# Kernel optimization log

Hardware: AMD Instinct MI355X
Metric: run time of the kernel (lower is better)

## Reference

```python
import jax, jax.numpy as jnp
import numpy as np

N = 25000      # number of target nodes
K = 32         # sampled neighbor fanout
F_IN = 256
F_OUT = 256


def setup_inputs() -> dict:
    key = jax.random.key(0)
    k1, k2, k3, k4 = jax.random.split(key, 4)
    x = jax.random.normal(k1, (N, F_IN), dtype=jnp.float32)
    neigh = jax.random.randint(k2, (N, K), 0, N, dtype=jnp.int64)
    # Linear(in_feats, out_feats) parameters
    W = jax.random.normal(k3, (F_IN, F_OUT), dtype=jnp.float32) / np.sqrt(F_IN)
    b = jax.random.normal(k4, (F_OUT,), dtype=jnp.float32) * 0.01
    return {"x": x, "neigh": neigh, "W": W, "b": b}


def reference(x, neigh, W, b):
    # Gather neighbor features: [N, K, F_IN]
    h = x[neigh]
    # Linear + ReLU transform on each neighbor feature
    h = jax.nn.relu(jnp.einsum('nkf,fo->nko', h, W) + b)
    # Element-wise max-pool across the neighbor set -> [N, F_OUT]
    return jnp.max(h, axis=1)
```

## Files before the change

### kernel.cpp

```cpp
#include <hip/hip_runtime.h>
#include <hip/hip_bf16.h>

#define N_NODES 25000
#define KFAN    32
#define FIN     256
#define FOUT    256

typedef float  f32x4  __attribute__((ext_vector_type(4)));
typedef short  s16x8  __attribute__((ext_vector_type(8)));

__device__ __forceinline__ ushort f2bf(float f) {
    unsigned int u = __float_as_uint(f);
    u += 0x7fffu + ((u >> 16) & 1u);
    return (ushort)(u >> 16);
}
__device__ __forceinline__ unsigned int pack2(float a, float b) {
    return (unsigned int)f2bf(a) | ((unsigned int)f2bf(b) << 16);
}

__global__ __launch_bounds__(256) void transpose_w(
    const float* __restrict__ W, ushort* __restrict__ Wt)
{
    __shared__ float ls[32][33];
    const int bid = blockIdx.x;
    const int kt  = bid & 7;
    const int nt  = bid >> 3;
    const int t   = threadIdx.x;

    {
        int kl = t >> 3, n4 = (t & 7) * 4;
        float4 v = *(const float4*)(W + (size_t)(kt * 32 + kl) * FOUT + nt * 32 + n4);
        ls[kl][n4 + 0] = v.x; ls[kl][n4 + 1] = v.y;
        ls[kl][n4 + 2] = v.z; ls[kl][n4 + 3] = v.w;
    }
    __syncthreads();
    {
        int nl = t >> 3, k4 = (t & 7) * 4;
        ushort4 o;
        o.x = f2bf(ls[k4 + 0][nl]);
        o.y = f2bf(ls[k4 + 1][nl]);
        o.z = f2bf(ls[k4 + 2][nl]);
        o.w = f2bf(ls[k4 + 3][nl]);
        *(ushort4*)(Wt + (size_t)(nt * 32 + nl) * FIN + kt * 32 + k4) = o;
    }
}

__global__ __launch_bounds__(256) void gemm_mfma(
    const float*  __restrict__ x,
    const ushort* __restrict__ Wt,
    const float*  __restrict__ bias,
    ushort*       __restrict__ y)
{
    __shared__ ushort As[64][72];

    const int tid  = threadIdx.x;
    const int lane = tid & 63;
    const int wv   = tid >> 6;
    const int l16  = lane & 15;
    const int q    = lane >> 4;
    const int row0 = blockIdx.x * 64;
    const int n0   = blockIdx.y * 128 + wv * 32;

    f32x4 acc[4][2];
    #pragma unroll
    for (int i = 0; i < 4; ++i)
        #pragma unroll
        for (int j = 0; j < 2; ++j) acc[i][j] = (f32x4)0.f;

    const int r    = tid >> 2;
    const int kcol = (tid & 3) * 16;

    for (int kc = 0; kc < FIN; kc += 64) {
        float4 v0 = make_float4(0.f,0.f,0.f,0.f), v1 = v0, v2 = v0, v3 = v0;
        int gr = row0 + r;
        if (gr < N_NODES) {
            const float* p = x + (size_t)gr * FIN + kc + kcol;
            v0 = *(const float4*)p;
            v1 = *(const float4*)(p + 4);
            v2 = *(const float4*)(p + 8);
            v3 = *(const float4*)(p + 12);
        }
        uint4 pa, pb;
        pa.x = pack2(v0.x, v0.y); pa.y = pack2(v0.z, v0.w);
        pa.z = pack2(v1.x, v1.y); pa.w = pack2(v1.z, v1.w);
        pb.x = pack2(v2.x, v2.y); pb.y = pack2(v2.z, v2.w);
        pb.z = pack2(v3.x, v3.y); pb.w = pack2(v3.z, v3.w);
        *(uint4*)&As[r][kcol]     = pa;
        *(uint4*)&As[r][kcol + 8] = pb;
        __syncthreads();

        #pragma unroll
        for (int kk = 0; kk < 64; kk += 32) {
            const int k0 = kk + q * 8;
            s16x8 a[4], b[2];
            #pragma unroll
            for (int mt = 0; mt < 4; ++mt)
                a[mt] = *(const s16x8*)&As[mt * 16 + l16][k0];
            #pragma unroll
            for (int ct = 0; ct < 2; ++ct)
                b[ct] = *(const s16x8*)(Wt + (size_t)(n0 + ct * 16 + l16) * FIN + kc + k0);
            #pragma unroll
            for (int mt = 0; mt < 4; ++mt)
                #pragma unroll
                for (int ct = 0; ct < 2; ++ct)
                    acc[mt][ct] = __builtin_amdgcn_mfma_f32_16x16x32_bf16(a[mt], b[ct], acc[mt][ct], 0, 0, 0);
        }
        __syncthreads();
    }

    #pragma unroll
    for (int ct = 0; ct < 2; ++ct) {
        const int col = n0 + ct * 16 + l16;
        const float bv = bias[col];
        #pragma unroll
        for (int mt = 0; mt < 4; ++mt) {
            #pragma unroll
            for (int rr = 0; rr < 4; ++rr) {
                int row = row0 + mt * 16 + q * 4 + rr;
                if (row < N_NODES)
                    y[(size_t)row * FOUT + col] = f2bf(fmaxf(acc[mt][ct][rr] + bv, 0.f));
            }
        }
    }
}

__global__ __launch_bounds__(256) void pool_max(
    const ushort* __restrict__ y,
    const int*    __restrict__ neigh,
    float*        __restrict__ out)
{
    const int bid   = blockIdx.x;
    const int chunk = bid & 3;
    const int nb    = bid >> 2;
    const int tid   = threadIdx.x;
    const int lane  = tid & 63;
    const int g     = lane >> 3;
    const int gl    = lane & 7;
    const int wv    = tid >> 6;

    const int n  = nb * 32 + wv * 8 + g;
    const int nc = n < N_NODES ? n : N_NODES - 1;

    const int4 iv = *(const int4*)(neigh + (size_t)nc * KFAN + gl * 4);
    const int base8 = lane & 56;
    int ia[4] = {iv.x, iv.y, iv.z, iv.w};

    const ushort* yc = y + chunk * 64 + gl * 8;

    s16x8 acc = (s16x8)0;
    #pragma unroll
    for (int k = 0; k < KFAN; ++k) {
        int idx = __shfl(ia[k & 3], base8 + (k >> 2));
        s16x8 cur = *(const s16x8*)(yc + (size_t)idx * FOUT);
        acc = __builtin_elementwise_max(acc, cur);
    }

    if (n < N_NODES) {
        f32x4 o0, o1;
        o0.x = __uint_as_float(((unsigned int)(ushort)acc[0]) << 16);
        o0.y = __uint_as_float(((unsigned int)(ushort)acc[1]) << 16);
        o0.z = __uint_as_float(((unsigned int)(ushort)acc[2]) << 16);
        o0.w = __uint_as_float(((unsigned int)(ushort)acc[3]) << 16);
        o1.x = __uint_as_float(((unsigned int)(ushort)acc[4]) << 16);
        o1.y = __uint_as_float(((unsigned int)(ushort)acc[5]) << 16);
        o1.z = __uint_as_float(((unsigned int)(ushort)acc[6]) << 16);
        o1.w = __uint_as_float(((unsigned int)(ushort)acc[7]) << 16);
        float* op = out + (size_t)n * FOUT + chunk * 64 + gl * 8;
        __builtin_nontemporal_store(o0, (f32x4*)op);
        __builtin_nontemporal_store(o1, (f32x4*)(op + 4));
    }
}

extern "C" void kernel_launch(void* const* d_in, const int* in_sizes, int n_in,
                              void* d_out, int out_size, void* d_ws, size_t ws_size,
                              hipStream_t stream) {
    const float* x     = (const float*)d_in[0];
    const int*   neigh = (const int*)  d_in[1];
    const float* W     = (const float*)d_in[2];
    const float* bias  = (const float*)d_in[3];
    float*       out   = (float*)d_out;
    ushort*      y     = (ushort*)d_ws;
    ushort*      Wt    = (ushort*)d_out;

    transpose_w<<<64, 256, 0, stream>>>(W, Wt);

    dim3 g1((N_NODES + 63) / 64, 2);
    gemm_mfma<<<g1, 256, 0, stream>>>(x, Wt, bias, y);

    const int nblocks = ((N_NODES + 31) / 32) * 4;
    pool_max<<<nblocks, 256, 0, stream>>>(y, neigh, out);
}
```

Baseline: 117.7 us.

## Chunk-major intermediate layout, full-N GEMM tiles, and prefetched neighbor indices

The GEMM now loads each 64-row block of x once into shared memory across the full K=256 and computes all 256 output columns per block, so x is no longer read twice by two column blocks. The intermediate y is stored chunk-major (four 64-column slabs), so each pool block's gathers hit a compact region that fits caches better. The pool kernel issues all neighbor-index shuffles up front and reads indices with nontemporal loads, which lets the gather loads issue back to back. In exchange the GEMM uses more shared memory and accumulator registers per block, which may cut occupancy, and the y writes become 128-byte-strided scalar stores.

```diff
diff --git a/kernel.cpp b/kernel.cpp
--- a/kernel.cpp
+++ b/kernel.cpp
@@ -5,8 +5,10 @@
 #define KFAN    32
 #define FIN     256
 #define FOUT    256
+#define CHUNK_STRIDE (N_NODES * 64)
 
 typedef float  f32x4  __attribute__((ext_vector_type(4)));
+typedef int    i32x4  __attribute__((ext_vector_type(4)));
 typedef short  s16x8  __attribute__((ext_vector_type(8)));
 
 __device__ __forceinline__ ushort f2bf(float f) {
@@ -51,7 +53,7 @@
     const float*  __restrict__ bias,
     ushort*       __restrict__ y)
 {
-    __shared__ ushort As[64][72];
+    __shared__ ushort As[64][264];
 
     const int tid  = threadIdx.x;
     const int lane = tid & 63;
@@ -59,66 +61,57 @@
     const int l16  = lane & 15;
     const int q    = lane >> 4;
     const int row0 = blockIdx.x * 64;
-    const int n0   = blockIdx.y * 128 + wv * 32;
+    const int n0   = wv * 64;
 
-    f32x4 acc[4][2];
+    #pragma unroll
+    for (int i = 0; i < 16; ++i) {
+        int row = i * 4 + wv;
+        int gr  = row0 + row;
+        float4 v = make_float4(0.f, 0.f, 0.f, 0.f);
+        if (gr < N_NODES)
+            v = *(const float4*)(x + (size_t)gr * FIN + lane * 4);
+        uint2 pk;
+        pk.x = pack2(v.x, v.y);
+        pk.y = pack2(v.z, v.w);
+        *(uint2*)&As[row][lane * 4] = pk;
+    }
+    __syncthreads();
+
+    f32x4 acc[4][4];
     #pragma unroll
     for (int i = 0; i < 4; ++i)
         #pragma unroll
-        for (int j = 0; j < 2; ++j) acc[i][j] = (f32x4)0.f;
+        for (int j = 0; j < 4; ++j) acc[i][j] = (f32x4)0.f;
 
-    const int r    = tid >> 2;
-    const int kcol = (tid & 3) * 16;
-
-    for (int kc = 0; kc < FIN; kc += 64) {
-        float4 v0 = make_float4(0.f,0.f,0.f,0.f), v1 = v0, v2 = v0, v3 = v0;
-        int gr = row0 + r;
-        if (gr < N_NODES) {
-            const float* p = x + (size_t)gr * FIN + kc + kcol;
-            v0 = *(const float4*)p;
-            v1 = *(const float4*)(p + 4);
-            v2 = *(const float4*)(p + 8);
-            v3 = *(const float4*)(p + 12);
-        }
-        uint4 pa, pb;
-        pa.x = pack2(v0.x, v0.y); pa.y = pack2(v0.z, v0.w);
-        pa.z = pack2(v1.x, v1.y); pa.w = pack2(v1.z, v1.w);
-        pb.x = pack2(v2.x, v2.y); pb.y = pack2(v2.z, v2.w);
-        pb.z = pack2(v3.x, v3.y); pb.w = pack2(v3.z, v3.w);
-        *(uint4*)&As[r][kcol]     = pa;
-        *(uint4*)&As[r][kcol + 8] = pb;
-        __syncthreads();
-
+    #pragma unroll
+    for (int ks = 0; ks < 8; ++ks) {
+        const int k0 = ks * 32 + q * 8;
+        s16x8 a[4], b[4];
         #pragma unroll
-        for (int kk = 0; kk < 64; kk += 32) {
-            const int k0 = kk + q * 8;
-            s16x8 a[4], b[2];
+        for (int mt = 0; mt < 4; ++mt)
+            a[mt] = *(const s16x8*)&As[mt * 16 + l16][k0];
+        #pragma unroll
+        for (int ct = 0; ct < 4; ++ct)
+            b[ct] = *(const s16x8*)(Wt + (size_t)(n0 + ct * 16 + l16) * FIN + k0);
+        #pragma unroll
+        for (int mt = 0; mt < 4; ++mt)
             #pragma unroll
-            for (int mt = 0; mt < 4; ++mt)
-                a[mt] = *(const s16x8*)&As[mt * 16 + l16][k0];
-            #pragma unroll
-            for (int ct = 0; ct < 2; ++ct)
-                b[ct] = *(const s16x8*)(Wt + (size_t)(n0 + ct * 16 + l16) * FIN + kc + k0);
-            #pragma unroll
-            for (int mt = 0; mt < 4; ++mt)
-                #pragma unroll
-                for (int ct = 0; ct < 2; ++ct)
-                    acc[mt][ct] = __builtin_amdgcn_mfma_f32_16x16x32_bf16(a[mt], b[ct], acc[mt][ct], 0, 0, 0);
-        }
-        __syncthreads();
+            for (int ct = 0; ct < 4; ++ct)
+                acc[mt][ct] = __builtin_amdgcn_mfma_f32_16x16x32_bf16(a[mt], b[ct], acc[mt][ct], 0, 0, 0);
     }
 
     #pragma unroll
-    for (int ct = 0; ct < 2; ++ct) {
+    for (int ct = 0; ct < 4; ++ct) {
         const int col = n0 + ct * 16 + l16;
         const float bv = bias[col];
+        ushort* yc = y + (size_t)(col >> 6) * CHUNK_STRIDE + (col & 63);
         #pragma unroll
         for (int mt = 0; mt < 4; ++mt) {
             #pragma unroll
             for (int rr = 0; rr < 4; ++rr) {
                 int row = row0 + mt * 16 + q * 4 + rr;
                 if (row < N_NODES)
-                    y[(size_t)row * FOUT + col] = f2bf(fmaxf(acc[mt][ct][rr] + bv, 0.f));
+                    yc[(size_t)row * 64] = f2bf(fmaxf(acc[mt][ct][rr] + bv, 0.f));
             }
         }
     }
@@ -141,17 +134,22 @@
     const int n  = nb * 32 + wv * 8 + g;
     const int nc = n < N_NODES ? n : N_NODES - 1;
 
-    const int4 iv = *(const int4*)(neigh + (size_t)nc * KFAN + gl * 4);
+    const i32x4 iv = __builtin_nontemporal_load(
+        (const i32x4*)(neigh + (size_t)nc * KFAN + gl * 4));
     const int base8 = lane & 56;
     int ia[4] = {iv.x, iv.y, iv.z, iv.w};
 
-    const ushort* yc = y + chunk * 64 + gl * 8;
+    int idx[KFAN];
+    #pragma unroll
+    for (int k = 0; k < KFAN; ++k)
+        idx[k] = __shfl(ia[k & 3], base8 + (k >> 2));
+
+    const ushort* yc = y + (size_t)chunk * CHUNK_STRIDE + gl * 8;
 
     s16x8 acc = (s16x8)0;
     #pragma unroll
     for (int k = 0; k < KFAN; ++k) {
-        int idx = __shfl(ia[k & 3], base8 + (k >> 2));
-        s16x8 cur = *(const s16x8*)(yc + (size_t)idx * FOUT);
+        s16x8 cur = *(const s16x8*)(yc + (size_t)idx[k] * 64);
         acc = __builtin_elementwise_max(acc, cur);
     }
 
@@ -184,8 +182,8 @@
 
     transpose_w<<<64, 256, 0, stream>>>(W, Wt);
 
-    dim3 g1((N_NODES + 63) / 64, 2);
-    gemm_mfma<<<g1, 256, 0, stream>>>(x, Wt, bias, y);
+    const int mblocks = (N_NODES + 63) / 64;
+    gemm_mfma<<<mblocks, 256, 0, stream>>>(x, Wt, bias, y);
 
     const int nblocks = ((N_NODES + 31) / 32) * 4;
     pool_max<<<nblocks, 256, 0, stream>>>(y, neigh, out);
```

Result: slower. 128.2 us (+8.9%).
